# Optimization experiments

Hardware: AMD Instinct MI355X
Metric: run time of the kernel (lower is better)

The kernel has to match this reference:

```python
import jax, jax.numpy as jnp
import numpy as np

D_MODEL = 512
N_HEADS = 8
D_HEAD = D_MODEL // N_HEADS


def setup_inputs() -> dict:
    key = jax.random.key(0)
    ks = jax.random.split(key, 11)
    B, S = 2, 4096
    scale = 1.0 / np.sqrt(D_MODEL)
    inp = {
        "q": jax.random.normal(ks[0], (B, S, D_MODEL), dtype=jnp.float32),
        "k": jax.random.normal(ks[1], (B, S, D_MODEL), dtype=jnp.float32),
        "v": jax.random.normal(ks[2], (B, S, D_MODEL), dtype=jnp.float32),
        "Wq": jax.random.normal(ks[3], (D_MODEL, D_MODEL), dtype=jnp.float32) * scale,
        "bq": jnp.zeros((D_MODEL,), dtype=jnp.float32),
        "Wk": jax.random.normal(ks[4], (D_MODEL, D_MODEL), dtype=jnp.float32) * scale,
        "bk": jnp.zeros((D_MODEL,), dtype=jnp.float32),
        "Wv": jax.random.normal(ks[5], (D_MODEL, D_MODEL), dtype=jnp.float32) * scale,
        "bv": jnpp if False else jnp.zeros((D_MODEL,), dtype=jnp.float32),
        "Wo": jax.random.normal(ks[6], (D_MODEL, D_MODEL), dtype=jnp.float32) * scale,
        "bo": jnp.zeros((D_MODEL,), dtype=jnp.float32),
    }
    return inp


def reference(q, k, v, Wq, bq, Wk, bk, Wv, bv, Wo, bo):
    B, S, _ = q.shape
    # Linear projections (torch Linear: x @ W^T + b), split into heads -> [B,H,S,Dh]
    def proj(x, W, b):
        y = jnp.einsum("bsd,ed->bse", x, W) + b
        return y.reshape(B, -1, N_HEADS, D_HEAD).transpose(0, 2, 1, 3)

    Q = proj(q, Wq, bq)
    K = proj(k, Wk, bk)
    V = proj(v, Wv, bv)

    inv_sqrt_dh = 1.0 / np.sqrt(D_HEAD).astype(np.float32)
    scores = jnp.einsum("bhqd,bhkd->bhqk", Q, K) * inv_sqrt_dh  # [B,H,S,S]
    attn = jax.nn.softmax(scores, axis=-1)  # dropout is identity at eval
    out = jnp.einsum("bhqk,bhkd->bhqd", attn, V)  # [B,H,S,Dh]
    out = out.transpose(0, 2, 1, 3).reshape(B, S, D_MODEL)
    return jnp.einsum("bsd,ed->bse", out, Wo) + bo
```

## Files before the change

kernel.cpp:

```cpp
#include <hip/hip_runtime.h>
#include <hip/hip_bf16.h>
#include <hip/hip_fp16.h>
#include <stdint.h>

#define D_MODEL 512
#define NH 8
#define DH 64
#define BB 2
#define SS 4096
#define MTOT (BB*SS)
#define NJQ 2

typedef __attribute__((ext_vector_type(8))) short bf16x8;
typedef __attribute__((ext_vector_type(4))) float f32x4;
typedef __fp16 fp16x2 __attribute__((ext_vector_type(2)));

#define MFMA32(a,b,c) __builtin_amdgcn_mfma_f32_16x16x32_bf16(a,b,c,0,0,0)

#if __has_builtin(__builtin_amdgcn_exp2f)
  #define EXP2F(x) __builtin_amdgcn_exp2f(x)
#else
  #define EXP2F(x) __expf((x) * 0.6931471805599453f)
#endif

#define QSCALE 0.18033688011112042f
#define EXPOFF 11.541560327679939f

__device__ __forceinline__ unsigned f2b(float f) {
  return (__float_as_uint(f) + 0x8000u) >> 16;
}
__device__ __forceinline__ float h2f(unsigned short h) {
  return __half2float(__ushort_as_half(h));
}
__device__ __forceinline__ unsigned packh2(float lo, float hi) {
  fp16x2 h = __builtin_amdgcn_cvt_pkrtz(lo, hi);
  return __builtin_bit_cast(unsigned, h);
}
__device__ __forceinline__ unsigned packpair(float lo, float hi) {
  return __builtin_amdgcn_perm(__float_as_uint(hi) + 0x8000u,
                               __float_as_uint(lo) + 0x8000u, 0x07060302u);
}
__device__ __forceinline__ unsigned cvtpk_bf16(float lo, float hi) {
  unsigned r;
  asm("v_cvt_pk_bf16_f32 %0, %1, %2" : "=v"(r) : "v"(lo), "v"(hi));
  return r;
}
__device__ __forceinline__ void gload_lds16(const unsigned short* g, unsigned short* l) {
  __builtin_amdgcn_global_load_lds(
      (const __attribute__((address_space(1))) unsigned int*)g,
      (__attribute__((address_space(3))) unsigned int*)l, 16, 0, 0);
}

struct PrepArgs {
  const float* src[7];
  unsigned short* dst[7];
  int off[8];
};

__global__ __launch_bounds__(256) void prep_kernel(PrepArgs a) {
  const int bx = blockIdx.x;
  int tgt = 0;
#pragma unroll
  for (int s = 1; s < 7; s++) tgt += (bx >= a.off[s]);
  const int i = ((bx - a.off[tgt]) * 256 + threadIdx.x) * 4;
  const float4 f = *(const float4*)(a.src[tgt] + i);
  uint2 o;
  o.x = packpair(f.x, f.y);
  o.y = packpair(f.z, f.w);
  *(uint2*)(a.dst[tgt] + i) = o;
}

struct CombArgs {
  const unsigned short* Os[NJQ];
  const float* ls[NJQ];
  unsigned short* Ao;
};

__global__ __launch_bounds__(256) void combine_kernel(CombArgs c) {
  const size_t i = ((size_t)blockIdx.x * 256 + threadIdx.x) * 8;
  const int m = (int)(i >> 9);
  const int k = (int)(i & 511);
  const int hh = k >> 6;
  float lsum = 0.f;
#pragma unroll
  for (int s = 0; s < NJQ; s++) lsum += c.ls[s][(size_t)m * NH + hh];
  const float inv = __builtin_amdgcn_rcpf(lsum);
  float sum[8] = {0.f, 0.f, 0.f, 0.f, 0.f, 0.f, 0.f, 0.f};
#pragma unroll
  for (int s = 0; s < NJQ; s++) {
    uint4 hv = *(const uint4*)(c.Os[s] + i);
    const unsigned short* he = (const unsigned short*)&hv;
#pragma unroll
    for (int e = 0; e < 8; e++) sum[e] += h2f(he[e]);
  }
  uint4 pk;
  pk.x = packpair(sum[0] * inv, sum[1] * inv);
  pk.y = packpair(sum[2] * inv, sum[3] * inv);
  pk.z = packpair(sum[4] * inv, sum[5] * inv);
  pk.w = packpair(sum[6] * inv, sum[7] * inv);
  *(uint4*)(c.Ao + i) = pk;
}

struct GemmArgs {
  const unsigned short* A[3];
  const unsigned short* W[3];
  const float* bias[3];
  unsigned short* out[3];
  float* outf;
  int mode;
};

__global__ __launch_bounds__(256) void gemm_kernel(GemmArgs g) {
  const int z = blockIdx.z;
  const float* __restrict__ bias = g.bias[z];
  unsigned short* __restrict__ out = g.out[z];
  const bool vt = (g.mode == 0) && (z == 2);
  const float osc = (g.mode == 0 && z == 0) ? QSCALE : 1.0f;

  __shared__ __align__(128) unsigned short lA[128][64];
  __shared__ __align__(128) unsigned short lB[128][64];

  const int t = threadIdx.x;
  const int lane = t & 63;
  const int w = t >> 6;
  const int wr = w >> 1, wc = w & 1;
  const int lrow = lane & 15, quad = lane >> 4;
  const int m0 = blockIdx.y * 128;
  const int n0 = blockIdx.x * 128;

  const int srow = lane >> 3;
  const int schunk = (lane & 7) * 8;

  const unsigned short* __restrict__ Ag = g.A[z];
  const unsigned short* __restrict__ Wg = g.W[z];

  f32x4 acc[4][4];
  for (int i = 0; i < 4; i++)
    for (int j = 0; j < 4; j++)
      for (int r = 0; r < 4; r++) acc[i][j][r] = 0.f;

  for (int kk = 0; kk < 512; kk += 64) {
#pragma unroll
    for (int i = 0; i < 4; i++) {
      const int r0 = w * 32 + i * 8;
      gload_lds16(Ag + (size_t)(m0 + r0 + srow) * 512 + kk + schunk, &lA[r0][0]);
      gload_lds16(Wg + (size_t)(n0 + r0 + srow) * 512 + kk + schunk, &lB[r0][0]);
    }
    __syncthreads();
#pragma unroll
    for (int ks = 0; ks < 2; ks++) {
      bf16x8 af[4], bfr[4];
#pragma unroll
      for (int mt = 0; mt < 4; mt++)
        af[mt] = *(const bf16x8*)&lA[wr * 64 + mt * 16 + lrow][ks * 32 + quad * 8];
#pragma unroll
      for (int nt = 0; nt < 4; nt++)
        bfr[nt] = *(const bf16x8*)&lB[wc * 64 + nt * 16 + lrow][ks * 32 + quad * 8];
#pragma unroll
      for (int mt = 0; mt < 4; mt++)
#pragma unroll
        for (int nt = 0; nt < 4; nt++)
          acc[mt][nt] = MFMA32(af[mt], bfr[nt], acc[mt][nt]);
    }
    __syncthreads();
  }

  float bv[4];
#pragma unroll
  for (int nt = 0; nt < 4; nt++) bv[nt] = bias[n0 + wc * 64 + nt * 16 + lrow];

#pragma unroll
  for (int mt = 0; mt < 4; mt++) {
#pragma unroll
    for (int nt = 0; nt < 4; nt++) {
      const int n = n0 + wc * 64 + nt * 16 + lrow;
      const int mB = m0 + wr * 64 + mt * 16 + quad * 4;
      float val[4];
#pragma unroll
      for (int r = 0; r < 4; r++) val[r] = (acc[mt][nt][r] + bv[nt]) * osc;

      if (g.mode == 1) {
#pragma unroll
        for (int r = 0; r < 4; r++) g.outf[(size_t)(mB + r) * 512 + n] = val[r];
      } else if (vt) {
        const int bb = mB >> 12, s = mB & 4095;
        const int a = s >> 2;
        const int c0 = (s & ~31) + (a & 4) + ((a & 3) << 3);
        const int hh = n >> 6, dh = n & 63;
        ushort4 pk = make_ushort4((unsigned short)f2b(val[0]), (unsigned short)f2b(val[1]),
                                  (unsigned short)f2b(val[2]), (unsigned short)f2b(val[3]));
        *(ushort4*)(out + (((size_t)bb * NH + hh) * DH + dh) * SS + c0) = pk;
      } else {
        const int bb = mB >> 12;
        const int hh = n >> 6, dh = n & 63;
#pragma unroll
        for (int r = 0; r < 4; r++) {
          const int s = (mB + r) & 4095;
          out[((((size_t)bb * NH + hh) * SS + s) << 6) + dh] = (unsigned short)f2b(val[r]);
        }
      }
    }
  }
}

struct AttnArgs {
  const unsigned short* Qh;
  const unsigned short* Kh;
  const unsigned short* Vt;
  unsigned short* Op[NJQ];
  float* lp[NJQ];
};

__global__ __launch_bounds__(512, 4) void attn_kernel(AttnArgs a) {
  __shared__ __align__(16) unsigned short lK[64][72];
  __shared__ __align__(16) unsigned short lV[64][72];

  const int t = threadIdx.x;
  const int lane = t & 63;
  const int w = t >> 6;
  const int lrow = lane & 15, quad = lane >> 4;
  const int h = blockIdx.y, b = blockIdx.z;
  const int qtile = blockIdx.x & 15, jq = blockIdx.x >> 4;
  const size_t kb = ((size_t)b * NH + h) * SS * DH;
  const size_t vb = ((size_t)b * NH + h) * DH * SS;
  const int qrow0 = qtile * 256 + w * 32;
  unsigned short* __restrict__ Op = a.Op[jq];
  float* __restrict__ lp = a.lp[jq];
  const int jt0 = jq * 32, jt1 = jt0 + 32;

  bf16x8 qf[2][2];
#pragma unroll
  for (int ti = 0; ti < 2; ti++) {
    const unsigned short* qp = a.Qh + kb + (size_t)(qrow0 + ti * 16 + lrow) * DH + quad * 8;
    qf[ti][0] = *(const bf16x8*)qp;
    qf[ti][1] = *(const bf16x8*)(qp + 32);
  }

  f32x4 o[2][4];
  float lsum[2] = {0.f, 0.f};
#pragma unroll
  for (int ti = 0; ti < 2; ti++)
    for (int nt = 0; nt < 4; nt++)
      for (int r = 0; r < 4; r++) o[ti][nt][r] = 0.f;

  const unsigned short* __restrict__ Kg = a.Kh + kb;
  const unsigned short* __restrict__ Vg = a.Vt + vb;

  const int rk = t >> 3;
  const int ck = (t & 7) * 8;

  uint4 kreg = *(const uint4*)(Kg + (size_t)(jt0 * 64 + rk) * DH + ck);
  uint4 vreg = *(const uint4*)(Vg + (size_t)rk * SS + jt0 * 64 + ck);

  const f32x4 sinit = {-EXPOFF, -EXPOFF, -EXPOFF, -EXPOFF};

  for (int jt = jt0; jt < jt1; jt++) {
    __syncthreads();
    *(uint4*)&lK[rk][ck] = kreg;
    *(uint4*)&lV[rk][ck] = vreg;
    {
      const int nb = (jt + 1 < jt1 ? jt + 1 : jt) * 64;
      kreg = *(const uint4*)(Kg + (size_t)(nb + rk) * DH + ck);
      vreg = *(const uint4*)(Vg + (size_t)rk * SS + nb + ck);
    }
    __syncthreads();

#pragma unroll
    for (int half = 0; half < 2; half++) {
      uint2 pw[2][2];
#pragma unroll
      for (int u = 0; u < 2; u++) {
        const int ntj = half * 2 + u;
        bf16x8 k0 = *(const bf16x8*)&lK[ntj * 16 + lrow][quad * 8];
        bf16x8 k1 = *(const bf16x8*)&lK[ntj * 16 + lrow][32 + quad * 8];
#pragma unroll
        for (int ti = 0; ti < 2; ti++) {
          f32x4 s = MFMA32(k0, qf[ti][0], sinit);
          s = MFMA32(k1, qf[ti][1], s);
          const float e0 = EXP2F(s[0]);
          const float e1 = EXP2F(s[1]);
          const float e2 = EXP2F(s[2]);
          const float e3 = EXP2F(s[3]);
          lsum[ti] += (e0 + e1) + (e2 + e3);
          pw[u][ti].x = cvtpk_bf16(e0, e1);
          pw[u][ti].y = cvtpk_bf16(e2, e3);
        }
      }
      bf16x8 pcat[2];
#pragma unroll
      for (int ti = 0; ti < 2; ti++) {
        uint4 c;
        c.x = pw[0][ti].x; c.y = pw[0][ti].y;
        c.z = pw[1][ti].x; c.w = pw[1][ti].y;
        pcat[ti] = __builtin_bit_cast(bf16x8, c);
      }
#pragma unroll
      for (int nt = 0; nt < 4; nt++) {
        bf16x8 vv = *(const bf16x8*)&lV[nt * 16 + lrow][half * 32 + quad * 8];
#pragma unroll
        for (int ti = 0; ti < 2; ti++)
          o[ti][nt] = MFMA32(vv, pcat[ti], o[ti][nt]);
      }
    }
  }

#pragma unroll
  for (int ti = 0; ti < 2; ti++) {
    float l = lsum[ti];
    l += __shfl_xor(l, 16);
    l += __shfl_xor(l, 32);
    const int si = qrow0 + ti * 16 + lrow;
    unsigned short* dst = Op + ((size_t)(b * SS + si)) * D_MODEL + h * DH;
#pragma unroll
    for (int nt = 0; nt < 4; nt++) {
      uint2 pk;
      pk.x = packh2(o[ti][nt][0], o[ti][nt][1]);
      pk.y = packh2(o[ti][nt][2], o[ti][nt][3]);
      *(uint2*)(dst + nt * 16 + quad * 4) = pk;
    }
    if (quad == 0)
      lp[(size_t)(b * SS + si) * NH + h] = l;
  }
}

extern "C" void kernel_launch(void* const* d_in, const int* in_sizes, int n_in,
                              void* d_out, int out_size, void* d_ws, size_t ws_size,
                              hipStream_t stream) {
  const float* q  = (const float*)d_in[0];
  const float* k  = (const float*)d_in[1];
  const float* v  = (const float*)d_in[2];
  const float* Wq = (const float*)d_in[3];
  const float* bq = (const float*)d_in[4];
  const float* Wk = (const float*)d_in[5];
  const float* bk = (const float*)d_in[6];
  const float* Wv = (const float*)d_in[7];
  const float* bv = (const float*)d_in[8];
  const float* Wo = (const float*)d_in[9];
  const float* bo = (const float*)d_in[10];

  const size_t NX = (size_t)MTOT * D_MODEL;
  const size_t NW = (size_t)D_MODEL * D_MODEL;

  char* p = (char*)d_ws;
  unsigned short* qb  = (unsigned short*)p; p += NX * 2;
  unsigned short* kbf = (unsigned short*)p; p += NX * 2;
  unsigned short* vbf = (unsigned short*)p; p += NX * 2;
  unsigned short* Wqb = (unsigned short*)p; p += NW * 2;
  unsigned short* Wkb = (unsigned short*)p; p += NW * 2;
  unsigned short* Wvb = (unsigned short*)p; p += NW * 2;
  unsigned short* Wob = (unsigned short*)p; p += NW * 2;
  unsigned short* Qh  = (unsigned short*)p; p += NX * 2;
  unsigned short* Kh  = (unsigned short*)p; p += NX * 2;
  unsigned short* Vtg = (unsigned short*)p; p += NX * 2;
  unsigned short* Ao  = (unsigned short*)p; p += NX * 2;
  unsigned short* Os[NJQ];
  float* ls[NJQ];
  for (int i = 0; i < NJQ; i++) { Os[i] = (unsigned short*)p; p += NX * 2; }
  for (int i = 0; i < NJQ; i++) { ls[i] = (float*)p; p += (size_t)MTOT * NH * 4; }

  PrepArgs pr;
  pr.src[0] = q;  pr.dst[0] = qb;
  pr.src[1] = k;  pr.dst[1] = kbf;
  pr.src[2] = v;  pr.dst[2] = vbf;
  pr.src[3] = Wq; pr.dst[3] = Wqb;
  pr.src[4] = Wk; pr.dst[4] = Wkb;
  pr.src[5] = Wv; pr.dst[5] = Wvb;
  pr.src[6] = Wo; pr.dst[6] = Wob;
  {
    const int nb[7] = {(int)(NX / 1024), (int)(NX / 1024), (int)(NX / 1024),
                       (int)(NW / 1024), (int)(NW / 1024), (int)(NW / 1024),
                       (int)(NW / 1024)};
    int acc = 0;
    for (int i = 0; i < 7; i++) { pr.off[i] = acc; acc += nb[i]; }
    pr.off[7] = acc;
    prep_kernel<<<dim3(acc, 1, 1), 256, 0, stream>>>(pr);
  }

  GemmArgs pa;
  pa.A[0] = qb; pa.A[1] = kbf; pa.A[2] = vbf;
  pa.W[0] = Wqb; pa.W[1] = Wkb; pa.W[2] = Wvb;
  pa.bias[0] = bq; pa.bias[1] = bk; pa.bias[2] = bv;
  pa.out[0] = Qh; pa.out[1] = Kh; pa.out[2] = Vtg;
  pa.outf = nullptr;
  pa.mode = 0;
  gemm_kernel<<<dim3(4, 64, 3), 256, 0, stream>>>(pa);

  AttnArgs aa;
  aa.Qh = Qh; aa.Kh = Kh; aa.Vt = Vtg;
  for (int i = 0; i < NJQ; i++) { aa.Op[i] = Os[i]; aa.lp[i] = ls[i]; }
  attn_kernel<<<dim3(16 * NJQ, NH, BB), 512, 0, stream>>>(aa);

  CombArgs ca;
  for (int i = 0; i < NJQ; i++) { ca.Os[i] = Os[i]; ca.ls[i] = ls[i]; }
  ca.Ao = Ao;
  combine_kernel<<<dim3((int)(NX / 8 / 256), 1, 1), 256, 0, stream>>>(ca);

  GemmArgs oa;
  oa.A[0] = Ao; oa.A[1] = Ao; oa.A[2] = Ao;
  oa.W[0] = Wob; oa.W[1] = Wob; oa.W[2] = Wob;
  oa.bias[0] = bo; oa.bias[1] = bo; oa.bias[2] = bo;
  oa.out[0] = nullptr; oa.out[1] = nullptr; oa.out[2] = nullptr;
  oa.outf = (float*)d_out;
  oa.mode = 1;
  gemm_kernel<<<dim3(4, 64, 1), 256, 0, stream>>>(oa);
}
```

Measured before the change: 234.0 us.

## Swap GEMM operand roles for vectorized row-major epilogue stores and halve K tile

For the non-V projections and the output projection, the MFMA operands are swapped so each lane's four accumulator values lie along the feature dimension. This lets the epilogue write contiguous ushort4/float4 vectors instead of four scalar strided stores per fragment, and load the bias as a vector. The K step per iteration also shrinks from 64 to 32, which halves LDS use per block and may raise occupancy, but it doubles the number of barrier-separated iterations.

```diff
diff --git a/kernel.cpp b/kernel.cpp
--- a/kernel.cpp
+++ b/kernel.cpp
@@ -117,8 +117,8 @@
   const bool vt = (g.mode == 0) && (z == 2);
   const float osc = (g.mode == 0 && z == 0) ? QSCALE : 1.0f;
 
-  __shared__ __align__(128) unsigned short lA[128][64];
-  __shared__ __align__(128) unsigned short lB[128][64];
+  __shared__ __align__(128) unsigned short lA[128][32];
+  __shared__ __align__(128) unsigned short lB[128][32];
 
   const int t = threadIdx.x;
   const int lane = t & 63;
@@ -128,61 +128,54 @@
   const int m0 = blockIdx.y * 128;
   const int n0 = blockIdx.x * 128;
 
-  const int srow = lane >> 3;
-  const int schunk = (lane & 7) * 8;
+  const int srow = lane >> 2;
+  const int schunk = (lane & 3) * 8;
 
   const unsigned short* __restrict__ Ag = g.A[z];
   const unsigned short* __restrict__ Wg = g.W[z];
+
+  const unsigned short (*pa)[32] = vt ? lA : lB;
+  const unsigned short (*pb)[32] = vt ? lB : lA;
 
   f32x4 acc[4][4];
   for (int i = 0; i < 4; i++)
     for (int j = 0; j < 4; j++)
       for (int r = 0; r < 4; r++) acc[i][j][r] = 0.f;
 
-  for (int kk = 0; kk < 512; kk += 64) {
-#pragma unroll
-    for (int i = 0; i < 4; i++) {
-      const int r0 = w * 32 + i * 8;
+  for (int kk = 0; kk < 512; kk += 32) {
+#pragma unroll
+    for (int i = 0; i < 2; i++) {
+      const int r0 = w * 32 + i * 16;
       gload_lds16(Ag + (size_t)(m0 + r0 + srow) * 512 + kk + schunk, &lA[r0][0]);
       gload_lds16(Wg + (size_t)(n0 + r0 + srow) * 512 + kk + schunk, &lB[r0][0]);
     }
     __syncthreads();
-#pragma unroll
-    for (int ks = 0; ks < 2; ks++) {
-      bf16x8 af[4], bfr[4];
-#pragma unroll
-      for (int mt = 0; mt < 4; mt++)
-        af[mt] = *(const bf16x8*)&lA[wr * 64 + mt * 16 + lrow][ks * 32 + quad * 8];
-#pragma unroll
-      for (int nt = 0; nt < 4; nt++)
-        bfr[nt] = *(const bf16x8*)&lB[wc * 64 + nt * 16 + lrow][ks * 32 + quad * 8];
-#pragma unroll
-      for (int mt = 0; mt < 4; mt++)
-#pragma unroll
-        for (int nt = 0; nt < 4; nt++)
-          acc[mt][nt] = MFMA32(af[mt], bfr[nt], acc[mt][nt]);
-    }
+    bf16x8 af[4], bfr[4];
+#pragma unroll
+    for (int a = 0; a < 4; a++) af[a] = *(const bf16x8*)&pa[wr * 64 + a * 16 + lrow][quad * 8];
+#pragma unroll
+    for (int b2 = 0; b2 < 4; b2++) bfr[b2] = *(const bf16x8*)&pb[wc * 64 + b2 * 16 + lrow][quad * 8];
+#pragma unroll
+    for (int a = 0; a < 4; a++)
+#pragma unroll
+      for (int b2 = 0; b2 < 4; b2++)
+        acc[a][b2] = MFMA32(af[a], bfr[b2], acc[a][b2]);
     __syncthreads();
   }
 
-  float bv[4];
-#pragma unroll
-  for (int nt = 0; nt < 4; nt++) bv[nt] = bias[n0 + wc * 64 + nt * 16 + lrow];
-
-#pragma unroll
-  for (int mt = 0; mt < 4; mt++) {
-#pragma unroll
-    for (int nt = 0; nt < 4; nt++) {
-      const int n = n0 + wc * 64 + nt * 16 + lrow;
-      const int mB = m0 + wr * 64 + mt * 16 + quad * 4;
-      float val[4];
-#pragma unroll
-      for (int r = 0; r < 4; r++) val[r] = (acc[mt][nt][r] + bv[nt]) * osc;
-
-      if (g.mode == 1) {
-#pragma unroll
-        for (int r = 0; r < 4; r++) g.outf[(size_t)(mB + r) * 512 + n] = val[r];
-      } else if (vt) {
+  if (vt) {
+    float bv[4];
+#pragma unroll
+    for (int nt = 0; nt < 4; nt++) bv[nt] = bias[n0 + wc * 64 + nt * 16 + lrow];
+#pragma unroll
+    for (int mt = 0; mt < 4; mt++) {
+#pragma unroll
+      for (int nt = 0; nt < 4; nt++) {
+        const int n = n0 + wc * 64 + nt * 16 + lrow;
+        const int mB = m0 + wr * 64 + mt * 16 + quad * 4;
+        float val[4];
+#pragma unroll
+        for (int r = 0; r < 4; r++) val[r] = acc[mt][nt][r] + bv[nt];
         const int bb = mB >> 12, s = mB & 4095;
         const int a = s >> 2;
         const int c0 = (s & ~31) + (a & 4) + ((a & 3) << 3);
@@ -190,13 +183,31 @@
         ushort4 pk = make_ushort4((unsigned short)f2b(val[0]), (unsigned short)f2b(val[1]),
                                   (unsigned short)f2b(val[2]), (unsigned short)f2b(val[3]));
         *(ushort4*)(out + (((size_t)bb * NH + hh) * DH + dh) * SS + c0) = pk;
-      } else {
-        const int bb = mB >> 12;
-        const int hh = n >> 6, dh = n & 63;
-#pragma unroll
-        for (int r = 0; r < 4; r++) {
-          const int s = (mB + r) & 4095;
-          out[((((size_t)bb * NH + hh) * SS + s) << 6) + dh] = (unsigned short)f2b(val[r]);
+      }
+    }
+  } else {
+    f32x4 bias4[4];
+#pragma unroll
+    for (int i = 0; i < 4; i++)
+      bias4[i] = *(const f32x4*)(bias + n0 + wr * 64 + i * 16 + quad * 4);
+#pragma unroll
+    for (int i = 0; i < 4; i++) {
+      const int nb = n0 + wr * 64 + i * 16 + quad * 4;
+#pragma unroll
+      for (int j = 0; j < 4; j++) {
+        const int m = m0 + wc * 64 + j * 16 + lrow;
+        float val[4];
+#pragma unroll
+        for (int r = 0; r < 4; r++) val[r] = (acc[i][j][r] + bias4[i][r]) * osc;
+        if (g.mode == 1) {
+          f32x4 v; v[0] = val[0]; v[1] = val[1]; v[2] = val[2]; v[3] = val[3];
+          *(f32x4*)(g.outf + (size_t)m * 512 + nb) = v;
+        } else {
+          const int bb = m >> 12, s = m & 4095;
+          const int hh = nb >> 6, dh = nb & 63;
+          ushort4 pk = make_ushort4((unsigned short)f2b(val[0]), (unsigned short)f2b(val[1]),
+                                    (unsigned short)f2b(val[2]), (unsigned short)f2b(val[3]));
+          *(ushort4*)(out + (((size_t)bb * NH + hh) * SS + s) * DH + dh) = pk;
         }
       }
     }
```

Measured after the change: 233.1 us. Within noise of the previous version (-0.4%).
